# Performance work log

Measured on AMD Instinct MI355X. Metric: run time of the kernel, lower is better.

Reference implementation:

```python
import jax, jax.numpy as jnp
import numpy as np

B, T, I, H, D = 256, 256, 64, 512, 256  # batch, seq_len, input_size, lstm_units, dense_units
R_ON = 0.05    # time-gate open ratio
ALPHA = 1e-3   # leak during closed phase
LN_EPS = 1e-5


def setup_inputs() -> dict:
    key = jax.random.key(0)
    ks = jax.random.split(key, 12)
    sc_in = 1.0 / np.sqrt(I)
    sc_h = 1.0 / np.sqrt(H)
    return {
        "x":  jax.random.normal(ks[0], (B, T, I), dtype=jnp.float32),
        # PLSTM weights (4 gates: i, f, g, o)
        "W":  jax.random.uniform(ks[1], (I, 4 * H), minval=-sc_in, maxval=sc_in, dtype=jnp.float32),
        "U":  jax.random.uniform(ks[2], (H, 4 * H), minval=-sc_h, maxval=sc_h, dtype=jnp.float32),
        "b":  jnp.zeros((4 * H,), dtype=jnp.float32),
        # Phased-LSTM time-gate parameters (per hidden unit)
        "tau": jnp.exp(jax.random.uniform(ks[3], (H,), minval=0.0, maxval=3.0, dtype=jnp.float32)),
        "s":   jax.random.uniform(ks[4], (H,), minval=0.0, maxval=10.0, dtype=jnp.float32),
        # LayerNorm
        "ln_gamma": jnp.ones((H,), dtype=jnp.float32),
        "ln_beta":  jnp.zeros((H,), dtype=jnp.float32),
        # Dense head
        "W1": jax.random.uniform(ks[5], (H, D), minval=-sc_h, maxval=sc_h, dtype=jnp.float32),
        "b1": jnp.zeros((D,), dtype=jnp.float32),
        "W2": jax.random.uniform(ks[6], (D, 1), minval=-1.0 / np.sqrt(D), maxval=1.0 / np.sqrt(D), dtype=jnp.float32),
        "b2": jnp.zeros((1,), dtype=jnp.float32),
    }


def _plstm_last_h(x, W, U, b, tau, s):
    # x: [B, T, I] -> last hidden state [B, H] of the phased LSTM
    xT = jnp.swapaxes(x, 0, 1)                 # [T, B, I]
    times = jnp.arange(x.shape[1], dtype=x.dtype)  # timestamps 0..T-1

    def step(carry, inp):
        h, c = carry
        x_t, t = inp
        z = x_t @ W + h @ U + b                # [B, 4H]
        i_g, f_g, g_g, o_g = jnp.split(z, 4, axis=-1)
        c_tilde = jax.nn.sigmoid(f_g) * c + jax.nn.sigmoid(i_g) * jnp.tanh(g_g)
        h_tilde = jax.nn.sigmoid(o_g) * jnp.tanh(c_tilde)
        # time gate k(t): piecewise-linear oscillation, per hidden unit
        phi = jnp.mod(t - s, tau) / tau        # [H]
        k = jnp.where(phi < 0.5 * R_ON, 2.0 * phi / R_ON,
             jnp.where(phi < R_ON, 2.0 - 2.0 * phi / R_ON, ALPHA * phi))
        c_new = k * c_tilde + (1.0 - k) * c
        h_new = k * h_tilde + (1.0 - k) * h
        return (h_new, c_new), None

    h0 = jnp.zeros((x.shape[0], tau.shape[0]), dtype=x.dtype)
    (h_last, _), _ = jax.lax.scan(step, (h0, h0), (xT, times))
    return h_last


def reference(x, W, U, b, tau, s, ln_gamma, ln_beta, W1, b1, W2, b2):
    h = _plstm_last_h(x, W, U, b, tau, s)      # [B, H] (== out[:, -1, :])
    # LayerNorm over hidden dim (per-position, so applying to last step is exact)
    mu = jnp.mean(h, axis=-1, keepdims=True)
    var = jnp.var(h, axis=-1, keepdims=True)
    hn = (h - mu) * jax.lax.rsqrt(var + LN_EPS) * ln_gamma + ln_beta
    # dropout layers are identity in eval mode
    out = hn @ W1 + b1
    out = out @ W2 + b2                        # [B, 1]
    return out
```

## Files before the change

kernel.cpp:

```cpp
#include <hip/hip_runtime.h>
#include <cmath>

#define NB 256
#define NT 512
#define NG 16
#define GB 16
#define B_ 256
#define T_ 256
#define I_ 64
#define H_ 512
#define G4H 2048
#define BT 16
#define UT 32
#define ZP 132
#define NFC 18
#define CPQ 17
#define CSTR 68
#define NCELL 1224
#define R_ON_F 0.05f
#define ALPHA_F 1.0e-3f
#define LN_EPS_F 1.0e-5f

typedef _Float16 h8 __attribute__((ext_vector_type(8)));
typedef _Float16 h4v __attribute__((ext_vector_type(4)));
typedef float f4 __attribute__((ext_vector_type(4)));
typedef float v4f __attribute__((ext_vector_type(4)));
typedef unsigned u4 __attribute__((ext_vector_type(4)));
typedef unsigned short us4 __attribute__((ext_vector_type(4)));

__device__ __align__(16) unsigned g_hp[2][B_ * H_];
__device__ __align__(16) float g_hf[B_ * H_];

struct alignas(256) PadCnt { unsigned v; unsigned pad[63]; };
__device__ PadCnt g_flag[NG][GB];
__device__ unsigned g_launch_cnt;

__device__ __forceinline__ float fast_sigmoid(float x) {
    return __builtin_amdgcn_rcpf(1.f + __expf(-x));
}
__device__ __forceinline__ float fast_tanh(float x) {
    return 1.f - 2.f * __builtin_amdgcn_rcpf(__expf(2.f * x) + 1.f);
}

struct HiLo { _Float16 hi, lo; };
__device__ __forceinline__ HiLo cvt_hilo(float v) {
    HiLo r;
    r.hi = (_Float16)v;
    r.lo = (_Float16)(v - (float)r.hi);
    return r;
}

__global__ __launch_bounds__(NT, 1) void plstm_scan_kernel(
    const float* __restrict__ x, const float* __restrict__ W,
    const float* __restrict__ U, const float* __restrict__ bias,
    const float* __restrict__ tau, const float* __restrict__ sph,
    const float* __restrict__ ln_g, const float* __restrict__ ln_b,
    const float* __restrict__ W1, const float* __restrict__ b1,
    const float* __restrict__ W2, const float* __restrict__ b2,
    float* __restrict__ out)
{
    __shared__ __align__(16) _Float16 Ah[NCELL * 8];
    __shared__ __align__(16) float zs[BT][ZP];
    __shared__ __align__(16) float kt[T_ * UT];
    __shared__ float red[16];
    __shared__ unsigned s_tag;

    const int tid = threadIdx.x;
    const int bt = blockIdx.x >> 4;
    const int ut = blockIdx.x & 15;
    const int b0 = bt * BT;
    const int u0 = ut * UT;

    if (tid == 0) s_tag = (atomicAdd(&g_launch_cnt, 1u) >> 8) + 1u;

    const int wv = tid >> 6;
    const int lane = tid & 63;
    const int n_ = lane & 15;
    const int q_ = lane >> 4;

    const int jg = (wv >> 1) * 512 + u0 + (wv & 1) * 16 + n_;
    h8 Bh[NFC], Bl[NFC];
    #pragma unroll
    for (int c = 0; c < NFC; ++c) {
        #pragma unroll
        for (int e = 0; e < 8; ++e) {
            const int kk = c * 32 + q_ * 8 + e;
            float v;
            if (c < 2) v = W[(size_t)kk * G4H + jg];
            else       v = U[(size_t)(kk - I_) * G4H + jg];
            const HiLo hl = cvt_hilo(v);
            Bh[c][e] = hl.hi;
            Bl[c][e] = hl.lo;
        }
    }
    const float bv = bias[jg];

    for (int idx = tid; idx < T_ * UT; idx += NT) {
        const int tt = idx >> 5, ul = idx & 31;
        const float ta = tau[u0 + ul];
        float aa = (float)tt - sph[u0 + ul];
        float rr = fmodf(aa, ta);
        if (rr < 0.f) rr += ta;
        const float phi = rr / ta;
        float kk;
        if (phi < 0.5f * R_ON_F)      kk = phi * (2.f / R_ON_F);
        else if (phi < R_ON_F)        kk = 2.f - phi * (2.f / R_ON_F);
        else                          kk = ALPHA_F * phi;
        kt[idx] = kk;
    }
    __syncthreads();
    const unsigned tagw = s_tag;
    const unsigned tagb = (tagw & 0xFFu) << 8;

    const int urow = tid >> 5;
    const int uu   = tid & 31;
    float c_st = 0.f;
    float h_st = 0.f;

    const int xr = (tid >> 4) & 15, xc4 = (tid & 15) << 2;
    const int cX = (tid & 15) >> 3, qX = ((tid & 15) >> 1) & 3;
    const int e0 = (tid & 1) << 2;
    const int fX = (cX * CSTR + qX * CPQ + xr) * 8 + e0;
    const int hr0 = tid >> 7, hk4 = (tid & 127) << 2;
    const int cS = 2 + ((tid & 127) >> 3), qS = ((tid & 127) >> 1) & 3;

    float4 xv = *(const float4*)(x + ((size_t)(b0 + xr) * T_ + 0) * I_ + xc4);

    const int fb = (q_ * CPQ + n_) * 8;

    int cur = 0;
    for (int t = 0; t < T_; ++t) {
        if (t == 0) {
            const h8 z8 = {};
            for (int idx = tid; idx < NCELL; idx += NT)
                *(h8*)&Ah[idx * 8] = z8;
            __syncthreads();
            if (tid < 256) {
                h4v xh;
                xh[0] = (_Float16)xv.x; xh[1] = (_Float16)xv.y;
                xh[2] = (_Float16)xv.z; xh[3] = (_Float16)xv.w;
                *(h4v*)&Ah[fX] = xh;
            }
        } else {
            const unsigned* hb = g_hp[cur] + (size_t)(b0 + hr0) * H_ + hk4;
            const unsigned want = tagb | (unsigned)t;
            u4 a0, a1, a2, a3;
            bool ok;
            do {
                asm volatile(
                    "global_load_dwordx4 %0, %4, off sc0 sc1\n\t"
                    "global_load_dwordx4 %1, %5, off sc0 sc1\n\t"
                    "global_load_dwordx4 %2, %6, off sc0 sc1\n\t"
                    "global_load_dwordx4 %3, %7, off sc0 sc1\n\t"
                    "s_waitcnt vmcnt(0)"
                    : "=&v"(a0), "=&v"(a1), "=&v"(a2), "=&v"(a3)
                    : "v"(hb), "v"(hb + 4 * H_), "v"(hb + 8 * H_), "v"(hb + 12 * H_)
                    : "memory");
                ok = ((a0[0] & 0xFFFFu) == want) & ((a0[1] & 0xFFFFu) == want)
                   & ((a0[2] & 0xFFFFu) == want) & ((a0[3] & 0xFFFFu) == want)
                   & ((a1[0] & 0xFFFFu) == want) & ((a1[1] & 0xFFFFu) == want)
                   & ((a1[2] & 0xFFFFu) == want) & ((a1[3] & 0xFFFFu) == want)
                   & ((a2[0] & 0xFFFFu) == want) & ((a2[1] & 0xFFFFu) == want)
                   & ((a2[2] & 0xFFFFu) == want) & ((a2[3] & 0xFFFFu) == want)
                   & ((a3[0] & 0xFFFFu) == want) & ((a3[1] & 0xFFFFu) == want)
                   & ((a3[2] & 0xFFFFu) == want) & ((a3[3] & 0xFFFFu) == want);
            } while (__ballot(!ok));
            const u4 av[4] = {a0, a1, a2, a3};
            #pragma unroll
            for (int it = 0; it < 4; ++it) {
                const int row = hr0 + 4 * it;
                const int fidx = (cS * CSTR + qS * CPQ + row) * 8 + e0;
                us4 uv;
                uv[0] = (unsigned short)(av[it][0] >> 16);
                uv[1] = (unsigned short)(av[it][1] >> 16);
                uv[2] = (unsigned short)(av[it][2] >> 16);
                uv[3] = (unsigned short)(av[it][3] >> 16);
                *(us4*)&Ah[fidx] = uv;
            }
        }
        __syncthreads();

        if (tid < 256) {
            const int tn = (t < T_ - 1) ? t + 1 : t;
            xv = *(const float4*)(x + ((size_t)(b0 + xr) * T_ + tn) * I_ + xc4);
        }

        f4 ac0 = {bv, bv, bv, bv};
        f4 ac1 = {0.f, 0.f, 0.f, 0.f};
        #pragma unroll
        for (int c = 0; c < NFC; ++c) {
            const h8 ah = *(const h8*)&Ah[fb + c * (CSTR * 8)];
            ac0 = __builtin_amdgcn_mfma_f32_16x16x32_f16(ah, Bh[c], ac0, 0, 0, 0);
            ac1 = __builtin_amdgcn_mfma_f32_16x16x32_f16(ah, Bl[c], ac1, 0, 0, 0);
        }
        const f4 zt = ac0 + ac1;
        {
            const int colz = wv * 16 + n_;
            const int rz = q_ * 4;
            zs[rz + 0][colz] = zt[0];
            zs[rz + 1][colz] = zt[1];
            zs[rz + 2][colz] = zt[2];
            zs[rz + 3][colz] = zt[3];
        }
        __syncthreads();

        {
            const float zi = zs[urow][uu];
            const float zf = zs[urow][32 + uu];
            const float zg = zs[urow][64 + uu];
            const float zo = zs[urow][96 + uu];
            const float si = fast_sigmoid(zi);
            const float sf = fast_sigmoid(zf);
            const float so = fast_sigmoid(zo);
            const float ct = sf * c_st + si * fast_tanh(zg);
            const float ht = so * fast_tanh(ct);
            const float kk = kt[(t << 5) + uu];
            const float hn = kk * ht + (1.f - kk) * h_st;
            c_st = kk * ct + (1.f - kk) * c_st;
            h_st = hn;
            if (t < T_ - 1) {
                const unsigned short hb16 = __builtin_bit_cast(unsigned short, (_Float16)hn);
                const unsigned packed = ((unsigned)hb16 << 16) | (tagb | (unsigned)(t + 1));
                unsigned* gp = g_hp[cur ^ 1] + (size_t)(b0 + urow) * H_ + (u0 + uu);
                asm volatile("global_store_dword %0, %1, off sc0 sc1"
                             :: "v"(gp), "v"(packed) : "memory");
            } else {
                float* gp = g_hf + (size_t)(b0 + urow) * H_ + (u0 + uu);
                asm volatile("global_store_dword %0, %1, off sc0 sc1\n\ts_waitcnt vmcnt(0)"
                             :: "v"(gp), "v"(hn) : "memory");
            }
        }

        if (t == T_ - 1) {
            __syncthreads();
            if (tid == 0) {
                unsigned fv = (tagw << 8) | 0xFFu;
                asm volatile("global_store_dword %0, %1, off sc0 sc1"
                             :: "v"(&g_flag[bt][ut].v), "v"(fv) : "memory");
            }
        }

        if (t < T_ - 1 && tid < 256) {
            h4v xh;
            xh[0] = (_Float16)xv.x; xh[1] = (_Float16)xv.y;
            xh[2] = (_Float16)xv.z; xh[3] = (_Float16)xv.w;
            *(h4v*)&Ah[fX] = xh;
        }
        cur ^= 1;
    }

    {
        if (tid < 64) {
            const unsigned want = (tagw << 8) | 0xFFu;
            const unsigned* fp = &g_flag[bt][tid & 15].v;
            unsigned v;
            do {
                asm volatile("global_load_dword %0, %1, off sc0 sc1\n\ts_waitcnt vmcnt(0)"
                             : "=v"(v) : "v"(fp) : "memory");
            } while (__ballot(v != want));
        }
        __syncthreads();

        const int r = b0 + ut;
        float hv;
        const float* hp = g_hf + (size_t)r * H_ + tid;
        asm volatile("global_load_dword %0, %1, off sc0 sc1\n\ts_waitcnt vmcnt(0)"
                     : "=v"(hv) : "v"(hp) : "memory");
        float s1 = hv, s2 = hv * hv;
        #pragma unroll
        for (int off = 32; off > 0; off >>= 1) {
            s1 += __shfl_down(s1, off, 64);
            s2 += __shfl_down(s2, off, 64);
        }
        const int ln = tid & 63;
        if (ln == 0) { red[wv] = s1; red[8 + wv] = s2; }
        __syncthreads();
        float S1 = 0.f, S2 = 0.f;
        #pragma unroll
        for (int w = 0; w < 8; ++w) { S1 += red[w]; S2 += red[8 + w]; }
        const float mu = S1 * (1.f / 512.f);
        const float var = S2 * (1.f / 512.f) - mu * mu;
        const float rstd = rsqrtf(var + LN_EPS_F);
        const float hn = (hv - mu) * rstd * ln_g[tid] + ln_b[tid];
        float w12 = 0.f;
        const float* w1p = W1 + (size_t)tid * 256;
        #pragma unroll 4
        for (int d = 0; d < 256; ++d) w12 = fmaf(w1p[d], W2[d], w12);
        float contrib = hn * w12;
        if (tid < 256) contrib = fmaf(b1[tid], W2[tid], contrib);
        #pragma unroll
        for (int off = 32; off > 0; off >>= 1) contrib += __shfl_down(contrib, off, 64);
        __syncthreads();
        if (ln == 0) red[wv] = contrib;
        __syncthreads();
        if (tid == 0) {
            float tot = b2[0];
            #pragma unroll
            for (int w = 0; w < 8; ++w) tot += red[w];
            out[r] = tot;
        }
    }
}

extern "C" void kernel_launch(void* const* d_in, const int* in_sizes, int n_in,
                              void* d_out, int out_size, void* d_ws, size_t ws_size,
                              hipStream_t stream) {
    const float* x   = (const float*)d_in[0];
    const float* W   = (const float*)d_in[1];
    const float* U   = (const float*)d_in[2];
    const float* b   = (const float*)d_in[3];
    const float* tau = (const float*)d_in[4];
    const float* s   = (const float*)d_in[5];
    const float* lng = (const float*)d_in[6];
    const float* lnb = (const float*)d_in[7];
    const float* W1  = (const float*)d_in[8];
    const float* b1  = (const float*)d_in[9];
    const float* W2  = (const float*)d_in[10];
    const float* b2  = (const float*)d_in[11];
    float* out = (float*)d_out;
    plstm_scan_kernel<<<dim3(NB), dim3(NT), 0, stream>>>(
        x, W, U, b, tau, s, lng, lnb, W1, b1, W2, b2, out);
}
```

Baseline: 763.0 us.

## Split hidden units across twice as many 256-thread blocks for the persistent scan

```diff
diff --git a/kernel.cpp b/kernel.cpp
--- a/kernel.cpp
+++ b/kernel.cpp
@@ -1,22 +1,23 @@
 #include <hip/hip_runtime.h>
 #include <cmath>
 
-#define NB 256
-#define NT 512
+#define NB 512
+#define NT 256
 #define NG 16
-#define GB 16
+#define GB 32
 #define B_ 256
 #define T_ 256
 #define I_ 64
 #define H_ 512
 #define G4H 2048
 #define BT 16
-#define UT 32
-#define ZP 132
+#define UT 16
+#define ZP 68
 #define NFC 18
 #define CPQ 17
 #define CSTR 68
 #define NCELL 1224
+#define KTN (T_ * UT)
 #define R_ON_F 0.05f
 #define ALPHA_F 1.0e-3f
 #define LN_EPS_F 1.0e-5f
@@ -24,7 +25,6 @@
 typedef _Float16 h8 __attribute__((ext_vector_type(8)));
 typedef _Float16 h4v __attribute__((ext_vector_type(4)));
 typedef float f4 __attribute__((ext_vector_type(4)));
-typedef float v4f __attribute__((ext_vector_type(4)));
 typedef unsigned u4 __attribute__((ext_vector_type(4)));
 typedef unsigned short us4 __attribute__((ext_vector_type(4)));
 
@@ -50,7 +50,7 @@
     return r;
 }
 
-__global__ __launch_bounds__(NT, 1) void plstm_scan_kernel(
+__global__ __launch_bounds__(NT, 2) void plstm_scan_kernel(
     const float* __restrict__ x, const float* __restrict__ W,
     const float* __restrict__ U, const float* __restrict__ bias,
     const float* __restrict__ tau, const float* __restrict__ sph,
@@ -61,24 +61,25 @@
 {
     __shared__ __align__(16) _Float16 Ah[NCELL * 8];
     __shared__ __align__(16) float zs[BT][ZP];
-    __shared__ __align__(16) float kt[T_ * UT];
+    __shared__ __align__(16) float kt[KTN];
     __shared__ float red[16];
     __shared__ unsigned s_tag;
+    __shared__ char padlds[16384];
 
     const int tid = threadIdx.x;
-    const int bt = blockIdx.x >> 4;
-    const int ut = blockIdx.x & 15;
+    const int bt = blockIdx.x >> 5;
+    const int ut = blockIdx.x & 31;
     const int b0 = bt * BT;
     const int u0 = ut * UT;
 
-    if (tid == 0) s_tag = (atomicAdd(&g_launch_cnt, 1u) >> 8) + 1u;
+    if (tid == 0) s_tag = (atomicAdd(&g_launch_cnt, 1u) >> 9) + 1u;
 
     const int wv = tid >> 6;
     const int lane = tid & 63;
     const int n_ = lane & 15;
     const int q_ = lane >> 4;
 
-    const int jg = (wv >> 1) * 512 + u0 + (wv & 1) * 16 + n_;
+    const int jg = wv * H_ + u0 + n_;
     h8 Bh[NFC], Bl[NFC];
     #pragma unroll
     for (int c = 0; c < NFC; ++c) {
@@ -95,8 +96,8 @@
     }
     const float bv = bias[jg];
 
-    for (int idx = tid; idx < T_ * UT; idx += NT) {
-        const int tt = idx >> 5, ul = idx & 31;
+    for (int idx = tid; idx < KTN; idx += NT) {
+        const int tt = idx >> 4, ul = idx & 15;
         const float ta = tau[u0 + ul];
         float aa = (float)tt - sph[u0 + ul];
         float rr = fmodf(aa, ta);
@@ -111,18 +112,22 @@
     __syncthreads();
     const unsigned tagw = s_tag;
     const unsigned tagb = (tagw & 0xFFu) << 8;
-
-    const int urow = tid >> 5;
-    const int uu   = tid & 31;
+    if (tagw == 0xFFFFFFFFu) padlds[0] = 1;
+
+    const int urow = tid >> 4;
+    const int uu   = tid & 15;
     float c_st = 0.f;
     float h_st = 0.f;
 
-    const int xr = (tid >> 4) & 15, xc4 = (tid & 15) << 2;
+    const int xr = tid >> 4, xc4 = (tid & 15) << 2;
     const int cX = (tid & 15) >> 3, qX = ((tid & 15) >> 1) & 3;
-    const int e0 = (tid & 1) << 2;
-    const int fX = (cX * CSTR + qX * CPQ + xr) * 8 + e0;
-    const int hr0 = tid >> 7, hk4 = (tid & 127) << 2;
-    const int cS = 2 + ((tid & 127) >> 3), qS = ((tid & 127) >> 1) & 3;
+    const int e0x = (tid & 1) << 2;
+    const int fX = (cX * CSTR + qX * CPQ + xr) * 8 + e0x;
+    const int m = tid & 127;
+    const int hr0 = tid >> 7;
+    const int hk4 = m << 2;
+    const int cS = 2 + (m >> 3), qS = (m >> 1) & 3;
+    const int e0 = (m & 1) << 2;
 
     float4 xv = *(const float4*)(x + ((size_t)(b0 + xr) * T_ + 0) * I_ + xc4);
 
@@ -135,7 +140,7 @@
             for (int idx = tid; idx < NCELL; idx += NT)
                 *(h8*)&Ah[idx * 8] = z8;
             __syncthreads();
-            if (tid < 256) {
+            {
                 h4v xh;
                 xh[0] = (_Float16)xv.x; xh[1] = (_Float16)xv.y;
                 xh[2] = (_Float16)xv.z; xh[3] = (_Float16)xv.w;
@@ -144,43 +149,47 @@
         } else {
             const unsigned* hb = g_hp[cur] + (size_t)(b0 + hr0) * H_ + hk4;
             const unsigned want = tagb | (unsigned)t;
-            u4 a0, a1, a2, a3;
+            u4 a0, a1, a2, a3, a4, a5, a6, a7;
             bool ok;
+            auto chk = [&](const u4& v) {
+                return ((v[0] & 0xFFFFu) == want) & ((v[1] & 0xFFFFu) == want)
+                     & ((v[2] & 0xFFFFu) == want) & ((v[3] & 0xFFFFu) == want);
+            };
             do {
                 asm volatile(
-                    "global_load_dwordx4 %0, %4, off sc0 sc1\n\t"
-                    "global_load_dwordx4 %1, %5, off sc0 sc1\n\t"
-                    "global_load_dwordx4 %2, %6, off sc0 sc1\n\t"
-                    "global_load_dwordx4 %3, %7, off sc0 sc1\n\t"
+                    "global_load_dwordx4 %0, %8, off sc0 sc1\n\t"
+                    "global_load_dwordx4 %1, %9, off sc0 sc1\n\t"
+                    "global_load_dwordx4 %2, %10, off sc0 sc1\n\t"
+                    "global_load_dwordx4 %3, %11, off sc0 sc1\n\t"
+                    "global_load_dwordx4 %4, %12, off sc0 sc1\n\t"
+                    "global_load_dwordx4 %5, %13, off sc0 sc1\n\t"
+                    "global_load_dwordx4 %6, %14, off sc0 sc1\n\t"
+                    "global_load_dwordx4 %7, %15, off sc0 sc1\n\t"
                     "s_waitcnt vmcnt(0)"
-                    : "=&v"(a0), "=&v"(a1), "=&v"(a2), "=&v"(a3)
-                    : "v"(hb), "v"(hb + 4 * H_), "v"(hb + 8 * H_), "v"(hb + 12 * H_)
+                    : "=&v"(a0), "=&v"(a1), "=&v"(a2), "=&v"(a3),
+                      "=&v"(a4), "=&v"(a5), "=&v"(a6), "=&v"(a7)
+                    : "v"(hb), "v"(hb + 2 * H_), "v"(hb + 4 * H_), "v"(hb + 6 * H_),
+                      "v"(hb + 8 * H_), "v"(hb + 10 * H_), "v"(hb + 12 * H_), "v"(hb + 14 * H_)
                     : "memory");
-                ok = ((a0[0] & 0xFFFFu) == want) & ((a0[1] & 0xFFFFu) == want)
-                   & ((a0[2] & 0xFFFFu) == want) & ((a0[3] & 0xFFFFu) == want)
-                   & ((a1[0] & 0xFFFFu) == want) & ((a1[1] & 0xFFFFu) == want)
-                   & ((a1[2] & 0xFFFFu) == want) & ((a1[3] & 0xFFFFu) == want)
-                   & ((a2[0] & 0xFFFFu) == want) & ((a2[1] & 0xFFFFu) == want)
-                   & ((a2[2] & 0xFFFFu) == want) & ((a2[3] & 0xFFFFu) == want)
-                   & ((a3[0] & 0xFFFFu) == want) & ((a3[1] & 0xFFFFu) == want)
-                   & ((a3[2] & 0xFFFFu) == want) & ((a3[3] & 0xFFFFu) == want);
+                ok = chk(a0) & chk(a1) & chk(a2) & chk(a3)
+                   & chk(a4) & chk(a5) & chk(a6) & chk(a7);
             } while (__ballot(!ok));
-            const u4 av[4] = {a0, a1, a2, a3};
+            const u4 av[8] = {a0, a1, a2, a3, a4, a5, a6, a7};
             #pragma unroll
-            for (int it = 0; it < 4; ++it) {
-                const int row = hr0 + 4 * it;
+            for (int i = 0; i < 8; ++i) {
+                const int row = hr0 + 2 * i;
                 const int fidx = (cS * CSTR + qS * CPQ + row) * 8 + e0;
                 us4 uv;
-                uv[0] = (unsigned short)(av[it][0] >> 16);
-                uv[1] = (unsigned short)(av[it][1] >> 16);
-                uv[2] = (unsigned short)(av[it][2] >> 16);
-                uv[3] = (unsigned short)(av[it][3] >> 16);
+                uv[0] = (unsigned short)(av[i][0] >> 16);
+                uv[1] = (unsigned short)(av[i][1] >> 16);
+                uv[2] = (unsigned short)(av[i][2] >> 16);
+                uv[3] = (unsigned short)(av[i][3] >> 16);
                 *(us4*)&Ah[fidx] = uv;
             }
         }
         __syncthreads();
 
-        if (tid < 256) {
+        {
             const int tn = (t < T_ - 1) ? t + 1 : t;
             xv = *(const float4*)(x + ((size_t)(b0 + xr) * T_ + tn) * I_ + xc4);
         }
@@ -206,15 +215,15 @@
 
         {
             const float zi = zs[urow][uu];
-            const float zf = zs[urow][32 + uu];
-            const float zg = zs[urow][64 + uu];
-            const float zo = zs[urow][96 + uu];
+            const float zf = zs[urow][16 + uu];
+            const float zg = zs[urow][32 + uu];
+            const float zo = zs[urow][48 + uu];
             const float si = fast_sigmoid(zi);
             const float sf = fast_sigmoid(zf);
             const float so = fast_sigmoid(zo);
             const float ct = sf * c_st + si * fast_tanh(zg);
             const float ht = so * fast_tanh(ct);
-            const float kk = kt[(t << 5) + uu];
+            const float kk = kt[(t << 4) + uu];
             const float hn = kk * ht + (1.f - kk) * h_st;
             c_st = kk * ct + (1.f - kk) * c_st;
             h_st = hn;
@@ -240,7 +249,7 @@
             }
         }
 
-        if (t < T_ - 1 && tid < 256) {
+        if (t < T_ - 1) {
             h4v xh;
             xh[0] = (_Float16)xv.x; xh[1] = (_Float16)xv.y;
             xh[2] = (_Float16)xv.z; xh[3] = (_Float16)xv.w;
@@ -249,10 +258,10 @@
         cur ^= 1;
     }
 
-    {
+    if (ut < 16) {
         if (tid < 64) {
             const unsigned want = (tagw << 8) | 0xFFu;
-            const unsigned* fp = &g_flag[bt][tid & 15].v;
+            const unsigned* fp = &g_flag[bt][tid & 31].v;
             unsigned v;
             do {
                 asm volatile("global_load_dword %0, %1, off sc0 sc1\n\ts_waitcnt vmcnt(0)"
@@ -262,11 +271,13 @@
         __syncthreads();
 
         const int r = b0 + ut;
-        float hv;
+        float hv0, hv1;
         const float* hp = g_hf + (size_t)r * H_ + tid;
-        asm volatile("global_load_dword %0, %1, off sc0 sc1\n\ts_waitcnt vmcnt(0)"
-                     : "=v"(hv) : "v"(hp) : "memory");
-        float s1 = hv, s2 = hv * hv;
+        asm volatile("global_load_dword %0, %2, off sc0 sc1\n\t"
+                     "global_load_dword %1, %3, off sc0 sc1\n\t"
+                     "s_waitcnt vmcnt(0)"
+                     : "=&v"(hv0), "=&v"(hv1) : "v"(hp), "v"(hp + 256) : "memory");
+        float s1 = hv0 + hv1, s2 = hv0 * hv0 + hv1 * hv1;
         #pragma unroll
         for (int off = 32; off > 0; off >>= 1) {
             s1 += __shfl_down(s1, off, 64);
@@ -277,17 +288,21 @@
         __syncthreads();
         float S1 = 0.f, S2 = 0.f;
         #pragma unroll
-        for (int w = 0; w < 8; ++w) { S1 += red[w]; S2 += red[8 + w]; }
+        for (int w = 0; w < 4; ++w) { S1 += red[w]; S2 += red[8 + w]; }
         const float mu = S1 * (1.f / 512.f);
         const float var = S2 * (1.f / 512.f) - mu * mu;
         const float rstd = rsqrtf(var + LN_EPS_F);
-        const float hn = (hv - mu) * rstd * ln_g[tid] + ln_b[tid];
-        float w12 = 0.f;
+        const float hn0 = (hv0 - mu) * rstd * ln_g[tid] + ln_b[tid];
+        const float hn1 = (hv1 - mu) * rstd * ln_g[tid + 256] + ln_b[tid + 256];
+        float w12a = 0.f, w12b = 0.f;
         const float* w1p = W1 + (size_t)tid * 256;
+        const float* w1q = W1 + (size_t)(tid + 256) * 256;
         #pragma unroll 4
-        for (int d = 0; d < 256; ++d) w12 = fmaf(w1p[d], W2[d], w12);
-        float contrib = hn * w12;
-        if (tid < 256) contrib = fmaf(b1[tid], W2[tid], contrib);
+        for (int d = 0; d < 256; ++d) {
+            w12a = fmaf(w1p[d], W2[d], w12a);
+            w12b = fmaf(w1q[d], W2[d], w12b);
+        }
+        float contrib = hn0 * w12a + hn1 * w12b + b1[tid] * W2[tid];
         #pragma unroll
         for (int off = 32; off > 0; off >>= 1) contrib += __shfl_down(contrib, off, 64);
         __syncthreads();
@@ -296,7 +311,7 @@
         if (tid == 0) {
             float tot = b2[0];
             #pragma unroll
-            for (int w = 0; w < 8; ++w) tot += red[w];
+            for (int w = 0; w < 4; ++w) tot += red[w];
             out[r] = tot;
         }
     }
```

After: 897.2 us. 17.6% more time.
